# Optimization experiments

Hardware: AMD Instinct MI355X
Metric: run time of the kernel (lower is better)

## Reference

```python
import jax, jax.numpy as jnp
import numpy as np

TOP_K = 30
NUM_RBF = 16
NUM_PE = 16
N_ATOMS = 14


def layer_norm(x, g, b, eps=1e-5):
    m = x.mean(-1, keepdims=True)
    v = ((x - m) ** 2).mean(-1, keepdims=True)
    return (x - m) / jnp.sqrt(v + eps) * g + b


def knn_idx(X_ca, mask):
    # pairwise CA distances, masked/adjusted, top-k smallest -> neighbor indices
    mask2D = mask[:, None, :] * mask[:, :, None]                    # [B,N,N]
    dX = X_ca[:, :, None, :] - X_ca[:, None, :, :]
    D = mask2D * jnp.sqrt((dX ** 2).sum(-1) + 1e-6)
    D_max = D.max(-1, keepdims=True)
    D_adjust = D + 2.0 * (1.0 - mask2D) * D_max
    _, E_idx = jax.lax.top_k(-D_adjust, TOP_K)                      # smallest distances
    return E_idx                                                     # [B,N,K]


def positional_encoding(E_idx):
    N_nodes = E_idx.shape[1]
    ii = jnp.arange(N_nodes, dtype=jnp.float32)[None, :, None]
    d = (E_idx.astype(jnp.float32) - ii)[..., None]                  # [B,N,K,1]
    freq = jnp.exp(jnp.arange(0, NUM_PE, 2, dtype=jnp.float32) * (-(np.log(10000.0) / NUM_PE)))
    ang = d * freq                                                   # [B,N,K,8]
    return jnp.concatenate([jnp.cos(ang), jnp.sin(ang)], -1)         # [B,N,K,16]


def setup_inputs():
    key = jax.random.key(0)
    ks = jax.random.split(key, 8)
    B, N = 1, 1024
    X = jax.random.normal(ks[0], (B, N, 14, 3), jnp.float32) * 3.0
    S = jax.random.randint(ks[1], (B, N), 0, 21)
    BB_D = jax.random.normal(ks[2], (B, N, 3, 2), jnp.float32)
    mask = jnp.ones((B, N), jnp.float32)
    node_in = 21 + 6                                 # one-hot(21) + sincos dihedrals(6)
    edge_in = NUM_PE + N_ATOMS * N_ATOMS * NUM_RBF   # 16 + 3136 = 3152
    node_w = jax.random.normal(ks[3], (node_in, 128), jnp.float32) * 0.05
    node_b = jnp.zeros((128,), jnp.float32)
    node_ln_g = jnp.ones((128,), jnp.float32)
    node_ln_b = jnp.zeros((128,), jnp.float32)
    edge_w = jax.random.normal(ks[4], (edge_in, 128), jnp.float32) * 0.02
    edge_b = jnp.zeros((128,), jnp.float32)
    edge_ln_g = jnp.ones((128,), jnp.float32)
    edge_ln_b = jnp.zeros((128,), jnp.float32)
    return {"X": X, "S": S, "BB_D": BB_D, "mask": mask,
            "node_w": node_w, "node_b": node_b, "node_ln_g": node_ln_g, "node_ln_b": node_ln_b,
            "edge_w": edge_w, "edge_b": edge_b, "edge_ln_g": edge_ln_g, "edge_ln_b": edge_ln_b}


def reference(X, S, BB_D, mask, node_w, node_b, node_ln_g, node_ln_b,
              edge_w, edge_b, edge_ln_g, edge_ln_b):
    X_ca = X[:, :, 1, :]
    E_idx = knn_idx(X_ca, mask)                                      # [B,N,K]
    E_pos = positional_encoding(E_idx)                               # [B,N,K,16]

    N_, Ca, C, O = X[:, :, 0], X[:, :, 1], X[:, :, 2], X[:, :, 3]
    b = Ca - N_
    c = C - Ca
    a = jnp.cross(b, c)
    Cb = -0.58273431 * a + 0.56802827 * b - 0.54067466 * c + Ca
    sc_atoms = X[..., 5:, :]                                         # 9 sidechain atoms
    Xa = jnp.concatenate([jnp.stack([N_, Ca, C, O, Cb], axis=-2), sc_atoms], axis=-2)  # [B,N,14,3]

    # gather neighbor atoms once, then all 14x14 atom-pair dists -> RBFs (same math as
    # the torch double loop over _get_rbf; loop order (i,j) == axes (A-atom, B-atom))
    X_nbr = jax.vmap(lambda xa, idx: xa[idx])(Xa, E_idx)             # [B,N,K,14,3]
    diff = Xa[:, :, None, :, None, :] - X_nbr[:, :, :, None, :, :]   # [B,N,K,14A,14B,3]
    Dab = jnp.sqrt((diff ** 2).sum(-1) + 1e-6)                       # [B,N,K,14,14]
    mu = jnp.linspace(0.0, 20.0, NUM_RBF)
    sigma = 20.0 / NUM_RBF
    RBF = jnp.exp(-(((Dab[..., None] - mu) / sigma) ** 2))           # [B,N,K,14,14,16]
    RBF_all = RBF.reshape(*RBF.shape[:3], -1)                        # [B,N,K,3136]

    E = jnp.concatenate([E_pos, RBF_all], -1)                        # [B,N,K,3152]

    V = jnp.concatenate([jax.nn.one_hot(S, 21, dtype=jnp.float32),
                         BB_D.reshape(*BB_D.shape[:-2], -1)], -1)    # [B,N,27]
    V = layer_norm(V @ node_w + node_b, node_ln_g, node_ln_b)
    E = layer_norm(E @ edge_w + edge_b, edge_ln_g, edge_ln_b)
    return V, E, E_idx
```

## Files before the change

### kernel.cpp

```cpp
#include <hip/hip_runtime.h>
#include <hip/hip_bf16.h>

#define TOPK 30
#define NAT 14
#define EDGE_IN 3152
#define NCHUNK 99
#define EPB 32
#define KSPLIT 50
#define WT2N (NCHUNK * 8 * 64)
#define WT2_BLOCKS ((WT2N + 255) / 256)

typedef __attribute__((ext_vector_type(8))) short bf16x8;
typedef __attribute__((ext_vector_type(4))) float f32x4;

__device__ __forceinline__ unsigned short f2bf(float f) {
    union { float f; unsigned u; } v; v.f = f;
    unsigned r = v.u + 0x7FFF + ((v.u >> 16) & 1);
    return (unsigned short)(r >> 16);
}
__device__ __forceinline__ float bf2f(unsigned short h) {
    union { unsigned u; float f; } v; v.u = ((unsigned)h) << 16;
    return v.f;
}
__device__ __forceinline__ short cvtbf(float f) {
    __hip_bfloat16 h = __float2bfloat16(f);
    return *reinterpret_cast<short*>(&h);
}

__global__ __launch_bounds__(256) void k_front(const float* __restrict__ X, const float* __restrict__ mask,
                                               int* __restrict__ Eidx, float* __restrict__ outI,
                                               float* __restrict__ Xa,
                                               const float* __restrict__ EW, unsigned short* __restrict__ Wt2,
                                               const int* __restrict__ S, const float* __restrict__ BB,
                                               const float* __restrict__ NW, const float* __restrict__ nb,
                                               const float* __restrict__ ng, const float* __restrict__ nbe,
                                               float* __restrict__ outV, int N) {
    __shared__ double sMax[4];
    __shared__ double sCd[128];
    __shared__ int    sCj[128];
    int b = blockIdx.x;
    if (b < N) {
        int i = b, t = threadIdx.x;
        int w = t >> 6, ln = t & 63;
        double mi = (double)mask[i];
        double xx = (double)X[((size_t)i * NAT + 1) * 3 + 0];
        double xy = (double)X[((size_t)i * NAT + 1) * 3 + 1];
        double xz = (double)X[((size_t)i * NAT + 1) * 3 + 2];
        double dv[4], m2v[4];
        double lmax = -1.0;
#pragma unroll
        for (int k = 0; k < 4; k++) {
            int j = w * 256 + ln + 64 * k;
            if (j < N) {
                double dx = xx - (double)X[((size_t)j * NAT + 1) * 3 + 0];
                double dy = xy - (double)X[((size_t)j * NAT + 1) * 3 + 1];
                double dz = xz - (double)X[((size_t)j * NAT + 1) * 3 + 2];
                double sq = ((dx * dx + dy * dy) + dz * dz) + 1e-6;
                double m2 = mi * (double)mask[j];
                double d = m2 * sqrt(sq);
                dv[k] = d; m2v[k] = m2;
                lmax = fmax(lmax, d);
            } else { dv[k] = 1e300; m2v[k] = 1.0; }
        }
#pragma unroll
        for (int m = 32; m; m >>= 1) lmax = fmax(lmax, __shfl_xor(lmax, m));
        if (ln == 0) sMax[w] = lmax;
        __syncthreads();
        double Dmax = fmax(fmax(sMax[0], sMax[1]), fmax(sMax[2], sMax[3]));
#pragma unroll
        for (int k = 0; k < 4; k++) {
            int j = w * 256 + ln + 64 * k;
            if (j < N) dv[k] = dv[k] + 2.0 * (1.0 - m2v[k]) * Dmax;
        }
        for (int s = 0; s < TOPK; s++) {
            double bd = dv[0]; int bj = w * 256 + ln;
            if (dv[1] < bd) { bd = dv[1]; bj = w * 256 + ln + 64; }
            if (dv[2] < bd) { bd = dv[2]; bj = w * 256 + ln + 128; }
            if (dv[3] < bd) { bd = dv[3]; bj = w * 256 + ln + 192; }
#pragma unroll
            for (int m = 32; m; m >>= 1) {
                double od = __shfl_xor(bd, m);
                int oj = __shfl_xor(bj, m);
                if (od < bd || (od == bd && oj < bj)) { bd = od; bj = oj; }
            }
            if (ln == 0) { sCd[w * TOPK + s] = bd; sCj[w * TOPK + s] = bj; }
            int rel = bj - w * 256 - ln;
            if (rel == 0)        dv[0] = 1e300;
            else if (rel == 64)  dv[1] = 1e300;
            else if (rel == 128) dv[2] = 1e300;
            else if (rel == 192) dv[3] = 1e300;
        }
        __syncthreads();
        if (w == 0) {
            double c0 = (ln < 4 * TOPK) ? sCd[ln] : 1e300;
            int    j0 = (ln < 4 * TOPK) ? sCj[ln] : 0x7FFFFFFF;
            int l1 = ln + 64;
            double c1 = (l1 < 4 * TOPK) ? sCd[l1] : 1e300;
            int    j1 = (l1 < 4 * TOPK) ? sCj[l1] : 0x7FFFFFFF;
            for (int s = 0; s < TOPK; s++) {
                double bd = c0; int bj = j0;
                if (c1 < bd || (c1 == bd && j1 < bj)) { bd = c1; bj = j1; }
#pragma unroll
                for (int m = 32; m; m >>= 1) {
                    double od = __shfl_xor(bd, m);
                    int oj = __shfl_xor(bj, m);
                    if (od < bd || (od == bd && oj < bj)) { bd = od; bj = oj; }
                }
                if (ln == 0) {
                    Eidx[(size_t)i * TOPK + s] = bj;
                    outI[(size_t)i * TOPK + s] = (float)bj;
                }
                if (j0 == bj) c0 = 1e300;
                if (j1 == bj) c1 = 1e300;
            }
        }
        return;
    }
    b -= N;
    if (b < WT2_BLOCKS) {
        int gid = b * 256 + threadIdx.x;
        if (gid >= WT2N) return;
        int ln = gid & 63;
        int kcf = gid >> 6;
        int kc = kcf >> 3, f = kcf & 7;
        int c = f * 16 + (ln & 15);
        int k0 = kc * 32 + (ln >> 4) * 8;
        bf16x8 o;
#pragma unroll
        for (int e = 0; e < 8; e++) {
            int k = k0 + e;
            float v = (k < EDGE_IN) ? EW[(size_t)k * 128 + c] : 0.f;
            o[e] = (short)f2bf(v);
        }
        *reinterpret_cast<bf16x8*>(Wt2 + (size_t)gid * 8) = o;
        return;
    }
    b -= WT2_BLOCKS;
    int prepBlocks = (N + 255) / 256;
    if (b < prepBlocks) {
        int i = b * 256 + threadIdx.x;
        if (i >= N) return;
        const float* xi = X + (size_t)i * NAT * 3;
        float* xo = Xa + (size_t)i * NAT * 3;
        float Nx = xi[0], Ny = xi[1], Nz = xi[2];
        float Ax = xi[3], Ay = xi[4], Az = xi[5];
        float Cx = xi[6], Cy = xi[7], Cz = xi[8];
        float bx = Ax - Nx, by = Ay - Ny, bz = Az - Nz;
        float cx = Cx - Ax, cy = Cy - Ay, cz = Cz - Az;
        float ax = by * cz - bz * cy;
        float ay = bz * cx - bx * cz;
        float az = bx * cy - by * cx;
        float Cbx = -0.58273431f * ax + 0.56802827f * bx - 0.54067466f * cx + Ax;
        float Cby = -0.58273431f * ay + 0.56802827f * by - 0.54067466f * cy + Ay;
        float Cbz = -0.58273431f * az + 0.56802827f * bz - 0.54067466f * cz + Az;
#pragma unroll
        for (int a = 0; a < 4; a++) { xo[a*3] = xi[a*3]; xo[a*3+1] = xi[a*3+1]; xo[a*3+2] = xi[a*3+2]; }
        xo[12] = Cbx; xo[13] = Cby; xo[14] = Cbz;
#pragma unroll
        for (int a = 5; a < 14; a++) { xo[a*3] = xi[a*3]; xo[a*3+1] = xi[a*3+1]; xo[a*3+2] = xi[a*3+2]; }
        return;
    }
    b -= prepBlocks;
    int i = b * 4 + (threadIdx.x >> 6);
    if (i >= N) return;
    int t = threadIdx.x & 63;
    int s = S[i];
    float b0 = BB[i*6], b1 = BB[i*6+1], b2 = BB[i*6+2], b3 = BB[i*6+3], b4 = BB[i*6+4], b5 = BB[i*6+5];
    int t2 = t + 64;
    float x0 = NW[(size_t)s*128 + t] + nb[t]
             + b0*NW[21*128+t] + b1*NW[22*128+t] + b2*NW[23*128+t]
             + b3*NW[24*128+t] + b4*NW[25*128+t] + b5*NW[26*128+t];
    float x1 = NW[(size_t)s*128 + t2] + nb[t2]
             + b0*NW[21*128+t2] + b1*NW[22*128+t2] + b2*NW[23*128+t2]
             + b3*NW[24*128+t2] + b4*NW[25*128+t2] + b5*NW[26*128+t2];
    float sum = x0 + x1;
#pragma unroll
    for (int m = 32; m; m >>= 1) sum += __shfl_xor(sum, m);
    float mean = sum * (1.f / 128.f);
    float d0 = x0 - mean, d1 = x1 - mean;
    float vs = d0*d0 + d1*d1;
#pragma unroll
    for (int m = 32; m; m >>= 1) vs += __shfl_xor(vs, m);
    float inv = 1.f / sqrtf(vs * (1.f / 128.f) + 1e-5f);
    outV[(size_t)i*128 + t]  = d0 * inv * ng[t]  + nbe[t];
    outV[(size_t)i*128 + t2] = d1 * inv * ng[t2] + nbe[t2];
}

__device__ __forceinline__ bf16x8 genA(int kb, float dpe, unsigned short du) {
    const float FR[8] = {1.0f, 0.31622776601683794f, 0.1f, 0.03162277660168379f,
                         0.01f, 0.0031622776601683794f, 0.001f, 0.00031622776601683794f};
    const float CS = 0.96089796f;
    const float CJ = 1.28119728f;
    bf16x8 a;
    if (kb < 16) {
#pragma unroll
        for (int jj = 0; jj < 8; jj++) {
            float ang = dpe * FR[jj];
            a[jj] = cvtbf((kb == 0) ? cosf(ang) : sinf(ang));
        }
    } else if (kb >= EDGE_IN) {
#pragma unroll
        for (int jj = 0; jj < 8; jj++) a[jj] = 0;
    } else {
        float D = bf2f(du);
        float bse = (float)((kb - 16) & 15);
        float Dss = D * CS - bse * CJ;
#pragma unroll
        for (int jj = 0; jj < 8; jj++) {
            float u = Dss - (float)jj * CJ;
            a[jj] = cvtbf(__builtin_amdgcn_exp2f(-u * u));
        }
    }
    return a;
}

__device__ __forceinline__ int idxD(int kc, int koff) {
    int idx = 2 * kc + (koff >> 1) - 1;
    return idx < 0 ? 0 : (idx > 195 ? 195 : idx);
}

__global__ __launch_bounds__(64) void k_edge(const float* __restrict__ Xa, const int* __restrict__ Eidx,
                                             const unsigned short* __restrict__ Wt2,
                                             float* __restrict__ P0, float* __restrict__ P1, int N) {
    __shared__ unsigned short sDh[EPB * 200];
    __shared__ float sDpe[EPB];
    const int NE = N * TOPK;
    int t = threadIdx.x;
    int eb = blockIdx.x >> 1, ks = blockIdx.x & 1;
    int geBase = eb * EPB;
    int kc0 = ks ? KSPLIT : 0;
    int kcEnd = ks ? NCHUNK : KSPLIT;
    float* Pdst = ks ? P1 : P0;

    const unsigned short* gB = Wt2 + (size_t)t * 8;

    bf16x8 bA[8], bB[8];
#pragma unroll
    for (int f = 0; f < 8; f++)
        bA[f] = *reinterpret_cast<const bf16x8*>(gB + ((size_t)kc0 * 8 + f) * 512);

    {
        int le = t >> 1, q = t & 1;
        int ge = geBase + le; if (ge >= NE) ge = NE - 1;
        int i = ge / TOPK;
        int j = Eidx[ge];
        if (q == 0) sDpe[le] = (float)j - (float)i;
        const float* Xi = Xa + (size_t)i * NAT * 3;
        const float* Xj = Xa + (size_t)j * NAT * 3;
        for (int p = q; p < 196; p += 2) {
            int a = p / 14, b = p - 14 * a;
            float dx = Xi[a*3+0] - Xj[b*3+0];
            float dy = Xi[a*3+1] - Xj[b*3+1];
            float dz = Xi[a*3+2] - Xj[b*3+2];
            sDh[le * 200 + p] = f2bf(sqrtf(dx*dx + dy*dy + dz*dz + 1e-6f));
        }
    }
    asm volatile("s_waitcnt lgkmcnt(0)" ::: "memory");

    int lrow = t & 15, koff = t >> 4;
    const unsigned short* sDrow0 = sDh + (size_t)lrow * 200;
    const unsigned short* sDrow1 = sDh + (size_t)(lrow + 16) * 200;
    float dpe0 = sDpe[lrow];
    float dpe1 = sDpe[lrow + 16];

    f32x4 acc0[8], acc1[8];
#pragma unroll
    for (int f = 0; f < 8; f++) { acc0[f] = (f32x4){0.f,0.f,0.f,0.f}; acc1[f] = (f32x4){0.f,0.f,0.f,0.f}; }

    int i0 = idxD(kc0, koff), i1 = idxD(kc0 + 1, koff), i2 = idxD(kc0 + 2, koff);
    unsigned short p0a = sDrow0[i0], p0b = sDrow1[i0];
    unsigned short p1a = sDrow0[i1], p1b = sDrow1[i1];
    unsigned short p2a = sDrow0[i2], p2b = sDrow1[i2];

    bf16x8 a0c = genA(kc0 * 32 + koff * 8, dpe0, p0a);
    bf16x8 a1c = genA(kc0 * 32 + koff * 8, dpe1, p0b);

    for (int kc = kc0; kc < kcEnd; kc += 2) {
        int i3 = idxD(kc + 3, koff);
        unsigned short p3a = sDrow0[i3], p3b = sDrow1[i3];
        bf16x8 a0n, a1n;
        if (kc + 1 < kcEnd) {
#pragma unroll
            for (int f = 0; f < 8; f++)
                bB[f] = *reinterpret_cast<const bf16x8*>(gB + ((size_t)(kc + 1) * 8 + f) * 512);
            int kb = (kc + 1) * 32 + koff * 8;
            a0n = genA(kb, dpe0, p1a);
            a1n = genA(kb, dpe1, p1b);
        }
#pragma unroll
        for (int f = 0; f < 8; f++) {
            acc0[f] = __builtin_amdgcn_mfma_f32_16x16x32_bf16(a0c, bA[f], acc0[f], 0, 0, 0);
            acc1[f] = __builtin_amdgcn_mfma_f32_16x16x32_bf16(a1c, bA[f], acc1[f], 0, 0, 0);
        }
        int i4 = idxD(kc + 4, koff);
        unsigned short p4a = sDrow0[i4], p4b = sDrow1[i4];
        if (kc + 2 < kcEnd) {
#pragma unroll
            for (int f = 0; f < 8; f++)
                bA[f] = *reinterpret_cast<const bf16x8*>(gB + ((size_t)(kc + 2) * 8 + f) * 512);
            int kb = (kc + 2) * 32 + koff * 8;
            a0c = genA(kb, dpe0, p2a);
            a1c = genA(kb, dpe1, p2b);
        }
        if (kc + 1 < kcEnd) {
#pragma unroll
            for (int f = 0; f < 8; f++) {
                acc0[f] = __builtin_amdgcn_mfma_f32_16x16x32_bf16(a0n, bB[f], acc0[f], 0, 0, 0);
                acc1[f] = __builtin_amdgcn_mfma_f32_16x16x32_bf16(a1n, bB[f], acc1[f], 0, 0, 0);
            }
        }
        p1a = p3a; p1b = p3b;
        p2a = p4a; p2b = p4b;
    }

#pragma unroll
    for (int g2 = 0; g2 < 2; g2++) {
#pragma unroll
        for (int r = 0; r < 4; r++) {
            int row = geBase + g2 * 16 + koff * 4 + r;
            if (row < NE) {
                float* po = Pdst + (size_t)row * 128 + lrow;
#pragma unroll
                for (int f = 0; f < 8; f++) po[f * 16] = (g2 ? acc1[f][r] : acc0[f][r]);
            }
        }
    }
}

__global__ __launch_bounds__(64) void k_lnred(const float* __restrict__ P0, const float* __restrict__ P1,
                                              const float* __restrict__ eb, const float* __restrict__ gg,
                                              const float* __restrict__ bb, float* __restrict__ outE) {
    int row = blockIdx.x, t = threadIdx.x;
    int c0 = t, c1 = t + 64;
    size_t base = (size_t)row * 128;
    float x0 = P0[base + c0] + P1[base + c0] + eb[c0];
    float x1 = P0[base + c1] + P1[base + c1] + eb[c1];
    float sum = x0 + x1;
#pragma unroll
    for (int m = 32; m; m >>= 1) sum += __shfl_xor(sum, m);
    float mean = sum * (1.f / 128.f);
    float d0 = x0 - mean, d1 = x1 - mean;
    float vs = d0*d0 + d1*d1;
#pragma unroll
    for (int m = 32; m; m >>= 1) vs += __shfl_xor(vs, m);
    float inv = 1.f / sqrtf(vs * (1.f / 128.f) + 1e-5f);
    outE[base + c0] = d0 * inv * gg[c0] + bb[c0];
    outE[base + c1] = d1 * inv * gg[c1] + bb[c1];
}

extern "C" void kernel_launch(void* const* d_in, const int* in_sizes, int n_in,
                              void* d_out, int out_size, void* d_ws, size_t ws_size,
                              hipStream_t stream) {
    const float* X       = (const float*)d_in[0];
    const int*   S       = (const int*)d_in[1];
    const float* BB      = (const float*)d_in[2];
    const float* mask    = (const float*)d_in[3];
    const float* node_w  = (const float*)d_in[4];
    const float* node_b  = (const float*)d_in[5];
    const float* node_g  = (const float*)d_in[6];
    const float* node_lb = (const float*)d_in[7];
    const float* edge_w  = (const float*)d_in[8];
    const float* edge_b  = (const float*)d_in[9];
    const float* edge_g  = (const float*)d_in[10];
    const float* edge_lb = (const float*)d_in[11];
    int N  = in_sizes[1];
    int NE = N * TOPK;

    float* out  = (float*)d_out;
    float* outV = out;
    float* outE = out + (size_t)N * 128;
    float* outI = outE + (size_t)NE * 128;

    char* ws = (char*)d_ws;
    int* Eidx = (int*)ws;
    size_t off = ((size_t)NE * 4 + 255) & ~(size_t)255;
    float* Xa = (float*)(ws + off);
    off += (((size_t)N * NAT * 3 * 4) + 255) & ~(size_t)255;
    unsigned short* Wt2 = (unsigned short*)(ws + off);
    off += ((size_t)WT2N * 8 * 2 + 255) & ~(size_t)255;
    float* P1 = (float*)(ws + off);

    int prepBlocks = (N + 255) / 256;
    int nodeBlocks = (N + 3) / 4;
    int frontBlocks = N + WT2_BLOCKS + prepBlocks + nodeBlocks;
    k_front<<<dim3(frontBlocks), dim3(256), 0, stream>>>(X, mask, Eidx, outI, Xa, edge_w, Wt2,
                                                         S, BB, node_w, node_b, node_g, node_lb, outV, N);
    k_edge<<<dim3(((NE + EPB - 1) / EPB) * 2), dim3(64), 0, stream>>>(Xa, Eidx, Wt2, outE, P1, N);
    k_lnred<<<dim3(NE), dim3(64), 0, stream>>>(outE, P1, edge_b, edge_g, edge_lb, outE);
}
```

Before: 133.6 us.

## Fuse split-K reduction and edge LayerNorm into edge kernel via atomic tickets

```diff
diff --git a/kernel.cpp b/kernel.cpp
--- a/kernel.cpp
+++ b/kernel.cpp
@@ -34,7 +34,8 @@
                                                const int* __restrict__ S, const float* __restrict__ BB,
                                                const float* __restrict__ NW, const float* __restrict__ nb,
                                                const float* __restrict__ ng, const float* __restrict__ nbe,
-                                               float* __restrict__ outV, int N) {
+                                               float* __restrict__ outV, int* __restrict__ ticket,
+                                               int nTick, int N) {
     __shared__ double sMax[4];
     __shared__ double sCd[128];
     __shared__ int    sCj[128];
@@ -161,29 +162,34 @@
         return;
     }
     b -= prepBlocks;
-    int i = b * 4 + (threadIdx.x >> 6);
-    if (i >= N) return;
-    int t = threadIdx.x & 63;
-    int s = S[i];
-    float b0 = BB[i*6], b1 = BB[i*6+1], b2 = BB[i*6+2], b3 = BB[i*6+3], b4 = BB[i*6+4], b5 = BB[i*6+5];
-    int t2 = t + 64;
-    float x0 = NW[(size_t)s*128 + t] + nb[t]
-             + b0*NW[21*128+t] + b1*NW[22*128+t] + b2*NW[23*128+t]
-             + b3*NW[24*128+t] + b4*NW[25*128+t] + b5*NW[26*128+t];
-    float x1 = NW[(size_t)s*128 + t2] + nb[t2]
-             + b0*NW[21*128+t2] + b1*NW[22*128+t2] + b2*NW[23*128+t2]
-             + b3*NW[24*128+t2] + b4*NW[25*128+t2] + b5*NW[26*128+t2];
-    float sum = x0 + x1;
-#pragma unroll
-    for (int m = 32; m; m >>= 1) sum += __shfl_xor(sum, m);
-    float mean = sum * (1.f / 128.f);
-    float d0 = x0 - mean, d1 = x1 - mean;
-    float vs = d0*d0 + d1*d1;
-#pragma unroll
-    for (int m = 32; m; m >>= 1) vs += __shfl_xor(vs, m);
-    float inv = 1.f / sqrtf(vs * (1.f / 128.f) + 1e-5f);
-    outV[(size_t)i*128 + t]  = d0 * inv * ng[t]  + nbe[t];
-    outV[(size_t)i*128 + t2] = d1 * inv * ng[t2] + nbe[t2];
+    int nodeBlocks = (N + 3) / 4;
+    if (b < nodeBlocks) {
+        int i = b * 4 + (threadIdx.x >> 6);
+        if (i >= N) return;
+        int t = threadIdx.x & 63;
+        int s = S[i];
+        float b0 = BB[i*6], b1 = BB[i*6+1], b2 = BB[i*6+2], b3 = BB[i*6+3], b4 = BB[i*6+4], b5 = BB[i*6+5];
+        int t2 = t + 64;
+        float x0 = NW[(size_t)s*128 + t] + nb[t]
+                 + b0*NW[21*128+t] + b1*NW[22*128+t] + b2*NW[23*128+t]
+                 + b3*NW[24*128+t] + b4*NW[25*128+t] + b5*NW[26*128+t];
+        float x1 = NW[(size_t)s*128 + t2] + nb[t2]
+                 + b0*NW[21*128+t2] + b1*NW[22*128+t2] + b2*NW[23*128+t2]
+                 + b3*NW[24*128+t2] + b4*NW[25*128+t2] + b5*NW[26*128+t2];
+        float sum = x0 + x1;
+#pragma unroll
+        for (int m = 32; m; m >>= 1) sum += __shfl_xor(sum, m);
+        float mean = sum * (1.f / 128.f);
+        float d0 = x0 - mean, d1 = x1 - mean;
+        float vs = d0*d0 + d1*d1;
+#pragma unroll
+        for (int m = 32; m; m >>= 1) vs += __shfl_xor(vs, m);
+        float inv = 1.f / sqrtf(vs * (1.f / 128.f) + 1e-5f);
+        outV[(size_t)i*128 + t]  = d0 * inv * ng[t]  + nbe[t];
+        outV[(size_t)i*128 + t2] = d1 * inv * ng[t2] + nbe[t2];
+        return;
+    }
+    for (int k = threadIdx.x; k < nTick; k += 256) ticket[k] = 0;
 }
 
 __device__ __forceinline__ bf16x8 genA(int kb, float dpe, unsigned short du) {
@@ -221,7 +227,11 @@
 
 __global__ __launch_bounds__(64) void k_edge(const float* __restrict__ Xa, const int* __restrict__ Eidx,
                                              const unsigned short* __restrict__ Wt2,
-                                             float* __restrict__ P0, float* __restrict__ P1, int N) {
+                                             float* __restrict__ P0, float* __restrict__ P1,
+                                             int* __restrict__ ticket,
+                                             const float* __restrict__ ebias, const float* __restrict__ egain,
+                                             const float* __restrict__ ebeta,
+                                             float* __restrict__ outE, int N) {
     __shared__ unsigned short sDh[EPB * 200];
     __shared__ float sDpe[EPB];
     const int NE = N * TOPK;
@@ -325,27 +335,44 @@
             }
         }
     }
-}
-
-__global__ __launch_bounds__(64) void k_lnred(const float* __restrict__ P0, const float* __restrict__ P1,
-                                              const float* __restrict__ eb, const float* __restrict__ gg,
-                                              const float* __restrict__ bb, float* __restrict__ outE) {
-    int row = blockIdx.x, t = threadIdx.x;
-    int c0 = t, c1 = t + 64;
-    size_t base = (size_t)row * 128;
-    float x0 = P0[base + c0] + P1[base + c0] + eb[c0];
-    float x1 = P0[base + c1] + P1[base + c1] + eb[c1];
-    float sum = x0 + x1;
-#pragma unroll
-    for (int m = 32; m; m >>= 1) sum += __shfl_xor(sum, m);
-    float mean = sum * (1.f / 128.f);
-    float d0 = x0 - mean, d1 = x1 - mean;
-    float vs = d0*d0 + d1*d1;
-#pragma unroll
-    for (int m = 32; m; m >>= 1) vs += __shfl_xor(vs, m);
-    float inv = 1.f / sqrtf(vs * (1.f / 128.f) + 1e-5f);
-    outE[base + c0] = d0 * inv * gg[c0] + bb[c0];
-    outE[base + c1] = d1 * inv * gg[c1] + bb[c1];
+    __threadfence();
+    int old = 0;
+    if (t == 0) old = atomicAdd(&ticket[eb], 1);
+    old = __shfl(old, 0);
+    if (old == 0) return;
+    __threadfence();
+
+    const float* Psrc = ks ? P0 : P1;
+    float gg[8], bb2[8], ebv[8];
+#pragma unroll
+    for (int f = 0; f < 8; f++) { int c = f * 16 + lrow; gg[f] = egain[c]; bb2[f] = ebeta[c]; ebv[f] = ebias[c]; }
+#pragma unroll
+    for (int g2 = 0; g2 < 2; g2++) {
+#pragma unroll
+        for (int r = 0; r < 4; r++) {
+            int row = geBase + g2 * 16 + koff * 4 + r;
+            if (row >= NE) continue;
+            const float* ps = Psrc + (size_t)row * 128 + lrow;
+            float x[8], sum = 0.f;
+#pragma unroll
+            for (int f = 0; f < 8; f++) {
+                float v = (g2 ? acc1[f][r] : acc0[f][r]) + ps[f * 16] + ebv[f];
+                x[f] = v; sum += v;
+            }
+#pragma unroll
+            for (int m = 1; m < 16; m <<= 1) sum += __shfl_xor(sum, m);
+            float mean = sum * (1.f / 128.f);
+            float vs = 0.f;
+#pragma unroll
+            for (int f = 0; f < 8; f++) { float d2 = x[f] - mean; vs += d2 * d2; }
+#pragma unroll
+            for (int m = 1; m < 16; m <<= 1) vs += __shfl_xor(vs, m);
+            float inv = 1.f / sqrtf(vs * (1.f / 128.f) + 1e-5f);
+            float* po = outE + (size_t)row * 128 + lrow;
+#pragma unroll
+            for (int f = 0; f < 8; f++) po[f * 16] = (x[f] - mean) * inv * gg[f] + bb2[f];
+        }
+    }
 }
 
 extern "C" void kernel_launch(void* const* d_in, const int* in_sizes, int n_in,
@@ -365,6 +392,7 @@
     const float* edge_lb = (const float*)d_in[11];
     int N  = in_sizes[1];
     int NE = N * TOPK;
+    int nTick = (NE + EPB - 1) / EPB;
 
     float* out  = (float*)d_out;
     float* outV = out;
@@ -378,13 +406,18 @@
     off += (((size_t)N * NAT * 3 * 4) + 255) & ~(size_t)255;
     unsigned short* Wt2 = (unsigned short*)(ws + off);
     off += ((size_t)WT2N * 8 * 2 + 255) & ~(size_t)255;
+    float* P0 = (float*)(ws + off);
+    off += (((size_t)NE * 128 * 4) + 255) & ~(size_t)255;
     float* P1 = (float*)(ws + off);
+    off += (((size_t)NE * 128 * 4) + 255) & ~(size_t)255;
+    int* ticket = (int*)(ws + off);
 
     int prepBlocks = (N + 255) / 256;
     int nodeBlocks = (N + 3) / 4;
-    int frontBlocks = N + WT2_BLOCKS + prepBlocks + nodeBlocks;
+    int frontBlocks = N + WT2_BLOCKS + prepBlocks + nodeBlocks + 1;
     k_front<<<dim3(frontBlocks), dim3(256), 0, stream>>>(X, mask, Eidx, outI, Xa, edge_w, Wt2,
-                                                         S, BB, node_w, node_b, node_g, node_lb, outV, N);
-    k_edge<<<dim3(((NE + EPB - 1) / EPB) * 2), dim3(64), 0, stream>>>(Xa, Eidx, Wt2, outE, P1, N);
-    k_lnred<<<dim3(NE), dim3(64), 0, stream>>>(outE, P1, edge_b, edge_g, edge_lb, outE);
-}
+                                                         S, BB, node_w, node_b, node_g, node_lb,
+                                                         outV, ticket, nTick, N);
+    k_edge<<<dim3(nTick * 2), dim3(64), 0, stream>>>(Xa, Eidx, Wt2, P0, P1, ticket,
+                                                     edge_b, edge_g, edge_lb, outE, N);
+}
```

Measured after the change: 266.5 us. +99.4%, slower.
